# Performance work log

Hardware: AMD Instinct MI355X
Metric: run time of the kernel (lower is better)

## Reference

```python
import jax, jax.numpy as jnp
import numpy as np

B, N, P, K = 64, 64, 128, 16

def setup_inputs() -> dict:
    key = jax.random.key(0)
    k1, k2, k3, k4 = jax.random.split(key, 4)
    x = jax.random.normal(k1, (B, N, P), dtype=jnp.float32)
    idx = jax.random.randint(k2, (B, P), 0, K)
    x_mask = jax.nn.one_hot(idx, K, dtype=jnp.float32)  # [B, P, K] one-hot
    # xavier_normal_ init for weights [K, N*N]
    std = float(np.sqrt(2.0 / (K + N * N)))
    weights = std * jax.random.normal(k3, (K, N * N), dtype=jnp.float32)
    g = jax.random.uniform(k4, (N * N, N * N), dtype=jnp.float32)
    return {"x": x, "x_mask": x_mask, "weights": weights, "g": g}

def reference(x, x_mask, weights, g):
    b, n, p = x.shape
    wg = jnp.matmul(weights ** 2, g)               # [K, N*N]
    w = jnp.einsum('bpk,km->bpm', x_mask, wg)      # [B, P, N*N]
    ef = jnp.exp(-w.reshape(b, p, n, n))           # [B, P, N, N]
    # torch does x[b].reshape(p, -1, 1): row-major reinterpretation of [N,P] -> [P,N]
    xr = x.reshape(b, p, n)                        # [B, P, N]
    Z = jnp.einsum('bpij,bpj->bi', ef, xr)         # batched matvec, summed over p
    return (Z, w)
```

## Files before the change

### kernel.cpp

```cpp
#include <hip/hip_runtime.h>
#include <hip/hip_bf16.h>


typedef float f32x4 __attribute__((ext_vector_type(4)));

__device__ __forceinline__ void dma16(const void* g, void* l) {
    __builtin_amdgcn_global_load_lds(
        (const __attribute__((address_space(1))) void*)g,
        (__attribute__((address_space(3))) void*)l, 16, 0, 0);
}

__global__ __launch_bounds__(256) void k_gemm(const float* __restrict__ W,
                                              const float* __restrict__ G,
                                              float* __restrict__ part) {
    __shared__ float buf[8192];
    float4* w2t4 = (float4*)buf;
    float4* stg  = (float4*)(buf + 4096);

    const int tc  = blockIdx.x & 15;
    const int mg  = blockIdx.x >> 4;
    const int tid = threadIdx.x;
    const int wv  = tid >> 6;
    const int ln  = tid & 63;
    const int tt  = tid >> 4;
    const int t0  = tc * 256;

    {
        float v[16];
#pragma unroll
        for (int k = 0; k < 16; ++k) {
            float w = W[k * 4096 + t0 + tid];
            v[k] = w * w;
        }
#pragma unroll
        for (int q = 0; q < 4; ++q) {
            const int slot = (q + (tid >> 1)) & 3;
            w2t4[tid * 4 + slot] =
                make_float4(v[4*q], v[4*q+1], v[4*q+2], v[4*q+3]);
        }
    }

    const float4* G4 = (const float4*)G;
    const int fi  = wv * 64 + ln;
    const int tl_ = fi >> 4;
    const int mc_ = fi & 15;

    dma16(&G4[(size_t)(t0 + tl_) * 1024 + mg * 16 + mc_], &stg[wv * 64]);
    __syncthreads();

    float4 acc[16];
#pragma unroll
    for (int k = 0; k < 16; ++k) acc[k] = make_float4(0.f, 0.f, 0.f, 0.f);

    for (int s = 0; s < 16; ++s) {
        if (s < 15)
            dma16(&G4[(size_t)(t0 + (s + 1) * 16 + tl_) * 1024 + mg * 16 + mc_],
                  &stg[((s + 1) & 1) * 256 + wv * 64]);

        const float4 g4 = stg[(s & 1) * 256 + tid];
        const int r = s * 16 + tt;
#pragma unroll
        for (int q = 0; q < 4; ++q) {
            const int slot = (q + (r >> 1)) & 3;
            const float4 wq = w2t4[r * 4 + slot];
            const float* wf = (const float*)&wq;
#pragma unroll
            for (int c = 0; c < 4; ++c) {
                const float sc = wf[c];
                acc[q*4+c].x = fmaf(sc, g4.x, acc[q*4+c].x);
                acc[q*4+c].y = fmaf(sc, g4.y, acc[q*4+c].y);
                acc[q*4+c].z = fmaf(sc, g4.z, acc[q*4+c].z);
                acc[q*4+c].w = fmaf(sc, g4.w, acc[q*4+c].w);
            }
        }
        __syncthreads();
    }

    float4* red = (float4*)buf;
    float4* p4  = (float4*)part;
#pragma unroll
    for (int r = 0; r < 2; ++r) {
#pragma unroll
        for (int ks = 0; ks < 8; ++ks)
            red[ks * 256 + tid] = acc[r * 8 + ks];
        __syncthreads();
        if (tid < 128) {
            const int ks = tid >> 4;
            const int c2 = tid & 15;
            float4 s = make_float4(0.f, 0.f, 0.f, 0.f);
#pragma unroll
            for (int t2 = 0; t2 < 16; ++t2) {
                float4 v = red[ks * 256 + t2 * 16 + c2];
                s.x += v.x; s.y += v.y; s.z += v.z; s.w += v.w;
            }
            const int k = r * 8 + ks;
            p4[(size_t)tc * 16384 + (size_t)k * 1024 + mg * 16 + c2] = s;
        }
        __syncthreads();
    }
}

__global__ __launch_bounds__(64) void k_reduce(const float* __restrict__ part,
                                               float* __restrict__ wg,
                                               float* __restrict__ E) {
    const int q = blockIdx.x * 64 + threadIdx.x;
    const float4* p4 = (const float4*)part;
    float4 s = make_float4(0.f, 0.f, 0.f, 0.f);
#pragma unroll
    for (int tc = 0; tc < 16; ++tc) {
        float4 v = p4[(size_t)tc * 16384 + q];
        s.x += v.x; s.y += v.y; s.z += v.z; s.w += v.w;
    }
    ((float4*)wg)[q] = s;
    ((float4*)E)[q] = make_float4(expf(-s.x), expf(-s.y), expf(-s.z), expf(-s.w));
}

__global__ __launch_bounds__(256) void k_wz(const float* __restrict__ x,
                                            const float* __restrict__ xmask,
                                            const float* __restrict__ wg,
                                            const float* __restrict__ E,
                                            float* __restrict__ wout,
                                            float* __restrict__ zout) {
    __shared__ float sw[4][16][64];
    __shared__ int   idx[128];
    __shared__ float zr[16][16];
    const int tid = threadIdx.x;
    const int wv  = tid >> 6;
    const int ln  = tid & 63;

    if (blockIdx.x < 2048) {
        const int bp0 = blockIdx.x * 4;
        const float* xm = xmask + (size_t)(bp0 + wv) * 16;
        float v = (ln < 16) ? xm[ln] : 0.f;
        unsigned long long bal = __ballot(v > 0.5f);
        if (ln == 0) idx[wv] = __ffsll((long long)bal) - 1;
        __syncthreads();
        const int k0 = idx[0], k1 = idx[1], k2 = idx[2], k3 = idx[3];
        const f32x4* s0 = (const f32x4*)(wg + (size_t)k0 * 4096);
        const f32x4* s1 = (const f32x4*)(wg + (size_t)k1 * 4096);
        const f32x4* s2 = (const f32x4*)(wg + (size_t)k2 * 4096);
        const f32x4* s3 = (const f32x4*)(wg + (size_t)k3 * 4096);
        f32x4* d = (f32x4*)(wout + (size_t)bp0 * 4096);
#pragma unroll
        for (int c = 0; c < 4; ++c) {
            const int o = c * 256 + tid;
            d[o]        = s0[o];
            d[1024 + o] = s1[o];
            d[2048 + o] = s2[o];
            d[3072 + o] = s3[o];
        }
        return;
    }

    const int zb = blockIdx.x - 2048;
    const int b  = zb >> 2;
    const int iq = zb & 3;

    if (tid < 128) {
        const float* xm = xmask + ((size_t)b * 128 + tid) * 16;
        int k = 0;
#pragma unroll
        for (int i = 0; i < 16; ++i) k = (xm[i] > 0.5f) ? i : k;
        idx[tid] = k;
    }
#pragma unroll
    for (int c = 0; c < 16; ++c)
        ((float*)sw)[c * 256 + tid] = 0.f;
    __syncthreads();

    const float* xb = x + (size_t)b * 8192;
    for (int p = wv * 32; p < wv * 32 + 32; ++p) {
        int k = idx[p];
        sw[wv][k][ln] += xb[p * 64 + ln];
    }
    __syncthreads();

    for (int e = tid; e < 1024; e += 256) {
        int k2 = e >> 6, j = e & 63;
        sw[0][k2][j] = sw[0][k2][j] + sw[1][k2][j] + sw[2][k2][j] + sw[3][k2][j];
    }
    __syncthreads();

    {
        const int k  = tid >> 4;
        const int il = tid & 15;
        const int i  = iq * 16 + il;
        float a = 0.f;
        const float4* Er = (const float4*)(E + (size_t)k * 4096 + i * 64);
        const float4* sr = (const float4*)(&sw[0][k][0]);
#pragma unroll
        for (int j4 = 0; j4 < 16; ++j4) {
            float4 e4 = Er[j4];
            float4 s4 = sr[j4];
            a = fmaf(e4.x, s4.x, a);
            a = fmaf(e4.y, s4.y, a);
            a = fmaf(e4.z, s4.z, a);
            a = fmaf(e4.w, s4.w, a);
        }
        zr[k][il] = a;
    }
    __syncthreads();
    if (tid < 16) {
        float s = 0.f;
#pragma unroll
        for (int k = 0; k < 16; ++k) s += zr[k][tid];
        zout[b * 64 + iq * 16 + tid] = s;
    }
}

extern "C" void kernel_launch(void* const* d_in, const int* in_sizes, int n_in,
                              void* d_out, int out_size, void* d_ws, size_t ws_size,
                              hipStream_t stream) {
    const float* x     = (const float*)d_in[0];
    const float* xmask = (const float*)d_in[1];
    const float* W     = (const float*)d_in[2];
    const float* G     = (const float*)d_in[3];

    float* zout = (float*)d_out;
    float* wout = (float*)d_out + 4096;

    float* wg = (float*)d_ws;
    float* E  = wg + 65536;

    float* part = wout;

    k_gemm  <<<1024, 256, 0, stream>>>(W, G, part);
    k_reduce<<<256,  64,  0, stream>>>(part, wg, E);
    k_wz    <<<2304, 256, 0, stream>>>(x, xmask, wg, E, wout, zout);
}
```

Measured before the change: 48.65 us.

## Move mask-index and x-bucketing work into extra blocks of the GEMM kernel

Adds extra blocks to the GEMM launch. They decode the one-hot mask into integer indices and pre-sum x rows per class into a global buffer, overlapping this work with the weight GEMM. The final kernel then reads the precomputed indices and per-class sums instead of redoing the ballot and shared-memory bucketing. The cost is extra global writes and reads of the intermediate buffers and more workspace use.

```diff
diff --git a/kernel.cpp b/kernel.cpp
--- a/kernel.cpp
+++ b/kernel.cpp
@@ -12,16 +12,54 @@
 
 __global__ __launch_bounds__(256) void k_gemm(const float* __restrict__ W,
                                               const float* __restrict__ G,
-                                              float* __restrict__ part) {
+                                              float* __restrict__ part,
+                                              const float* __restrict__ x,
+                                              const float* __restrict__ xmask,
+                                              float* __restrict__ sbuf,
+                                              int* __restrict__ idxg) {
     __shared__ float buf[8192];
-    float4* w2t4 = (float4*)buf;
-    float4* stg  = (float4*)(buf + 4096);
-
-    const int tc  = blockIdx.x & 15;
-    const int mg  = blockIdx.x >> 4;
     const int tid = threadIdx.x;
     const int wv  = tid >> 6;
     const int ln  = tid & 63;
+
+    if (blockIdx.x >= 1088) {
+        const int row = (blockIdx.x - 1088) * 256 + tid;
+        const float* xm = xmask + (size_t)row * 16;
+        int k = 0;
+#pragma unroll
+        for (int j = 0; j < 16; ++j) k = (xm[j] > 0.5f) ? j : k;
+        idxg[row] = k;
+        return;
+    }
+
+    if (blockIdx.x >= 1024) {
+        const int b = blockIdx.x - 1024;
+        float* sw  = buf;
+        int*  idxp = (int*)(buf + 4096);
+        if (tid < 128) {
+            const float* xm = xmask + ((size_t)b * 128 + tid) * 16;
+            int k = 0;
+#pragma unroll
+            for (int i = 0; i < 16; ++i) k = (xm[i] > 0.5f) ? i : k;
+            idxp[tid] = k;
+        }
+#pragma unroll
+        for (int c = 0; c < 16; ++c) sw[c * 256 + tid] = 0.f;
+        __syncthreads();
+        const float* xb = x + (size_t)b * 8192;
+        for (int p = wv * 32; p < wv * 32 + 32; ++p)
+            sw[wv * 1024 + idxp[p] * 64 + ln] += xb[p * 64 + ln];
+        __syncthreads();
+        for (int e = tid; e < 1024; e += 256)
+            sbuf[b * 1024 + e] = sw[e] + sw[1024 + e] + sw[2048 + e] + sw[3072 + e];
+        return;
+    }
+
+    float4* w2t4 = (float4*)buf;
+    float4* stg  = (float4*)(buf + 4096);
+
+    const int tc  = blockIdx.x & 15;
+    const int mg  = blockIdx.x >> 4;
     const int tt  = tid >> 4;
     const int t0  = tc * 256;
 
@@ -115,27 +153,21 @@
     ((float4*)E)[q] = make_float4(expf(-s.x), expf(-s.y), expf(-s.z), expf(-s.w));
 }
 
-__global__ __launch_bounds__(256) void k_wz(const float* __restrict__ x,
-                                            const float* __restrict__ xmask,
+__global__ __launch_bounds__(256) void k_wz(const int* __restrict__ idxg,
                                             const float* __restrict__ wg,
                                             const float* __restrict__ E,
+                                            const float* __restrict__ sbuf,
                                             float* __restrict__ wout,
                                             float* __restrict__ zout) {
-    __shared__ float sw[4][16][64];
-    __shared__ int   idx[128];
     __shared__ float zr[16][16];
     const int tid = threadIdx.x;
-    const int wv  = tid >> 6;
-    const int ln  = tid & 63;
 
     if (blockIdx.x < 2048) {
         const int bp0 = blockIdx.x * 4;
-        const float* xm = xmask + (size_t)(bp0 + wv) * 16;
-        float v = (ln < 16) ? xm[ln] : 0.f;
-        unsigned long long bal = __ballot(v > 0.5f);
-        if (ln == 0) idx[wv] = __ffsll((long long)bal) - 1;
-        __syncthreads();
-        const int k0 = idx[0], k1 = idx[1], k2 = idx[2], k3 = idx[3];
+        const int k0 = idxg[bp0 + 0];
+        const int k1 = idxg[bp0 + 1];
+        const int k2 = idxg[bp0 + 2];
+        const int k3 = idxg[bp0 + 3];
         const f32x4* s0 = (const f32x4*)(wg + (size_t)k0 * 4096);
         const f32x4* s1 = (const f32x4*)(wg + (size_t)k1 * 4096);
         const f32x4* s2 = (const f32x4*)(wg + (size_t)k2 * 4096);
@@ -155,39 +187,13 @@
     const int zb = blockIdx.x - 2048;
     const int b  = zb >> 2;
     const int iq = zb & 3;
-
-    if (tid < 128) {
-        const float* xm = xmask + ((size_t)b * 128 + tid) * 16;
-        int k = 0;
-#pragma unroll
-        for (int i = 0; i < 16; ++i) k = (xm[i] > 0.5f) ? i : k;
-        idx[tid] = k;
-    }
-#pragma unroll
-    for (int c = 0; c < 16; ++c)
-        ((float*)sw)[c * 256 + tid] = 0.f;
-    __syncthreads();
-
-    const float* xb = x + (size_t)b * 8192;
-    for (int p = wv * 32; p < wv * 32 + 32; ++p) {
-        int k = idx[p];
-        sw[wv][k][ln] += xb[p * 64 + ln];
-    }
-    __syncthreads();
-
-    for (int e = tid; e < 1024; e += 256) {
-        int k2 = e >> 6, j = e & 63;
-        sw[0][k2][j] = sw[0][k2][j] + sw[1][k2][j] + sw[2][k2][j] + sw[3][k2][j];
-    }
-    __syncthreads();
-
     {
         const int k  = tid >> 4;
         const int il = tid & 15;
         const int i  = iq * 16 + il;
         float a = 0.f;
         const float4* Er = (const float4*)(E + (size_t)k * 4096 + i * 64);
-        const float4* sr = (const float4*)(&sw[0][k][0]);
+        const float4* sr = (const float4*)(sbuf + (size_t)b * 1024 + k * 64);
 #pragma unroll
         for (int j4 = 0; j4 < 16; ++j4) {
             float4 e4 = Er[j4];
@@ -203,7 +209,7 @@
     if (tid < 16) {
         float s = 0.f;
 #pragma unroll
-        for (int k = 0; k < 16; ++k) s += zr[k][tid];
+        for (int kk = 0; kk < 16; ++kk) s += zr[kk][tid];
         zout[b * 64 + iq * 16 + tid] = s;
     }
 }
@@ -219,12 +225,14 @@
     float* zout = (float*)d_out;
     float* wout = (float*)d_out + 4096;
 
-    float* wg = (float*)d_ws;
-    float* E  = wg + 65536;
+    float* wg   = (float*)d_ws;
+    float* E    = wg + 65536;
+    float* sbuf = E + 65536;
+    int*   idxg = (int*)(sbuf + 65536);
 
     float* part = wout;
 
-    k_gemm  <<<1024, 256, 0, stream>>>(W, G, part);
+    k_gemm  <<<1120, 256, 0, stream>>>(W, G, part, x, xmask, sbuf, idxg);
     k_reduce<<<256,  64,  0, stream>>>(part, wg, E);
-    k_wz    <<<2304, 256, 0, stream>>>(x, xmask, wg, E, wout, zout);
-}
+    k_wz    <<<2304, 256, 0, stream>>>(idxg, wg, E, sbuf, wout, zout);
+}
```

Result: faster. 47.19 us (-3.0%).
